# Kernel tuning notes

Measured on AMD Instinct MI355X. Metric: run time of the kernel, lower is better.

Reference implementation:

```python
import jax, jax.numpy as jnp
import numpy as np

B, L, D, H = 2, 2048, 512, 8
Dh = D // H


def setup_inputs() -> dict:
    key = jax.random.key(0)
    ks = jax.random.split(key, 12)
    def lin(i):
        W = jax.random.normal(ks[i], (D, D), dtype=jnp.float32) * (1.0 / np.sqrt(D))
        b = jax.random.normal(ks[i + 1], (D,), dtype=jnp.float32) * 0.02
        return W, b
    Wq, bq = lin(0)
    Wk, bk = lin(2)
    Wv, bv = lin(4)
    Wo, bo = lin(6)
    wave_real = jax.random.normal(ks[8], (B, L, D), dtype=jnp.float32)
    wave_imag = jax.random.normal(ks[9], (B, L, D), dtype=jnp.float32)
    return {"wave_real": wave_real, "wave_imag": wave_imag,
            "Wq": Wq, "bq": bq, "Wk": Wk, "bk": bk,
            "Wv": Wv, "bv": bv, "Wo": Wo, "bo": bo}


def _heads(x):
    # (B,L,D) -> (B,H,L,Dh)
    return x.reshape(B, L, H, Dh).transpose(0, 2, 1, 3)


def reference(wave_real, wave_imag, Wq, bq, Wk, bk, Wv, bv, Wo, bo):
    Qr = _heads(wave_real @ Wq.T + bq)
    Qi = _heads(wave_imag @ Wq.T + bq)
    Kr = _heads(wave_real @ Wk.T + bk)
    Ki = _heads(wave_imag @ Wk.T + bk)
    Vr = _heads(wave_real @ Wv.T + bv)
    Vi = _heads(wave_imag @ Wv.T + bv)

    inner_real = jnp.einsum('bhid,bhjd->bhij', Qr, Kr) + jnp.einsum('bhid,bhjd->bhij', Qi, Ki)
    inner_imag = jnp.einsum('bhid,bhjd->bhij', Qr, Ki) - jnp.einsum('bhid,bhjd->bhij', Qi, Kr)

    scores = (inner_real ** 2 + inner_imag ** 2) / np.sqrt(Dh).astype(np.float32)
    attention = jax.nn.softmax(scores, axis=-1)

    phase = jnp.arctan2(inner_imag, inner_real)
    ac = attention * jnp.cos(phase)  # (B,H,L,L)
    as_ = attention * jnp.sin(phase)

    # sum_j att_ij*(Vr_j*cos_ij - Vi_j*sin_ij) -- fused contraction, same math as
    # the original's materialized (B,H,L,L,Dh) rotate-then-sum.
    out_real = jnp.einsum('bhij,bhjd->bhid', ac, Vr) - jnp.einsum('bhij,bhjd->bhid', as_, Vi)
    out_imag = jnp.einsum('bhij,bhjd->bhid', as_, Vr) + jnp.einsum('bhij,bhjd->bhid', ac, Vi)

    out_real = out_real.transpose(0, 2, 1, 3).reshape(B, L, D)
    out_imag = out_imag.transpose(0, 2, 1, 3).reshape(B, L, D)
    return (out_real @ Wo.T + bo, out_imag @ Wo.T + bo, attention)
```

## Files before the change

kernel.cpp:

```cpp
#include <hip/hip_runtime.h>

typedef unsigned short u16;
typedef unsigned int   u32;
typedef __attribute__((ext_vector_type(4)))  u16   us4;
typedef __attribute__((ext_vector_type(8)))  u16   us8;
typedef __attribute__((ext_vector_type(8)))  short s8v;
typedef __attribute__((ext_vector_type(16))) float f32x16;

#define L_   2048
#define D_   512
#define H_   8
#define PE_  2097152ull

#define MATE    2097152ull
#define BHE     131072u
#define VT_OFF  33554432ull
#define ORH_OFF 41943040ull
#define ORL_OFF 46137344ull
#define OIH_OFF 50331648ull
#define OIL_OFF 54525952ull
#define LV_OFF  58720256ull

#define XRH_O 16777216ull
#define XRL_O 20971520ull
#define XIH_O 25165824ull
#define XIL_O 29360128ull

#define MFMA32(a,b,c) __builtin_amdgcn_mfma_f32_32x32x16_bf16(a,b,c,0,0,0)
#define ROWOF(r,hi) (((r)&3) + 8*((r)>>2) + 4*(hi))

__device__ __forceinline__ u16 f2bf(float x){
    u32 u = __float_as_uint(x);
    u += 0x7FFFu + ((u>>16)&1u);
    return (u16)(u>>16);
}
__device__ __forceinline__ float bf2f(u16 h){ return __uint_as_float(((u32)h)<<16); }

__global__ __launch_bounds__(256)
void split_prep_kernel(const float* __restrict__ wr, const float* __restrict__ wi,
                       unsigned char* __restrict__ outb)
{
    const int z = blockIdx.y;
    const float* src = z ? wi : wr;
    u16* hg = (u16*)(outb + (z ? XIH_O : XRH_O));
    u16* lg = (u16*)(outb + (z ? XIL_O : XRL_O));
    const size_t idx4 = ((size_t)blockIdx.x * 256 + threadIdx.x) * 4;
    float4 v = *(const float4*)&src[idx4];
    float vv[4] = { v.x, v.y, v.z, v.w };
    us4 h, l;
    #pragma unroll
    for (int c = 0; c < 4; ++c) {
        u16 hb = f2bf(vv[c]);
        h[c] = hb;
        l[c] = f2bf(vv[c] - bf2f(hb));
    }
    *(us4*)&hg[idx4] = h;
    *(us4*)&lg[idx4] = l;
}

__device__ __forceinline__ s8v ldfrag(const unsigned char* Lp, u32 matOff, u32 row, u32 colb)
{
    return *(const s8v*)(Lp + matOff + row*128u + (colb ^ ((row&7u)<<4)));
}
__device__ __forceinline__ void stage_qk(unsigned char* Lp, u32 matOff,
                                         const u16* __restrict__ g, int rowBase, int tid)
{
    const int ch = tid & 7;
    const int r0 = tid >> 3;
    #pragma unroll
    for (int rr = 0; rr < 2; ++rr) {
        u32 row = rr*32 + r0;
        us8 v = ((const us8*)(g + (size_t)(rowBase + row)*64))[ch];
        *(us8*)(Lp + matOff + row*128u + (((u32)ch<<4) ^ ((row&7u)<<4))) = v;
    }
}
__device__ __forceinline__ void stage_vt(unsigned char* Lp, u32 matOff,
                                         const u16* __restrict__ g, int j0, int tid, bool neg)
{
    const int ch = tid & 7;
    const int r0 = tid >> 3;
    #pragma unroll
    for (int rr = 0; rr < 2; ++rr) {
        u32 dh = rr*32 + r0;
        us8 v = ((const us8*)(g + (size_t)dh*2048 + j0))[ch];
        if (neg) v = v ^ (u16)0x8000u;
        *(us8*)(Lp + matOff + dh*128u + (((u32)ch<<4) ^ ((dh&7u)<<4))) = v;
    }
}

__global__ __launch_bounds__(256, 2)
void proj_mfma_kernel(const unsigned char* __restrict__ scr,
                      const float* __restrict__ Wq, const float* __restrict__ Wk,
                      const float* __restrict__ Wv,
                      const float* __restrict__ bq, const float* __restrict__ bk,
                      const float* __restrict__ bv,
                      u16* __restrict__ qk, u16* __restrict__ vt)
{
    const int z = blockIdx.z;
    const u16* Ah_g = (const u16*)(scr + ((z & 1) ? XIH_O : XRH_O));
    const u16* Al_g = (const u16*)(scr + ((z & 1) ? XIL_O : XRL_O));
    const int wsel = z >> 1;
    const float* Wf; const float* bias;
    if (wsel == 0)      { Wf = Wq; bias = bq; }
    else if (wsel == 1) { Wf = Wk; bias = bk; }
    else                { Wf = Wv; bias = bv; }
    const bool four = (wsel < 2);

    const int m0 = blockIdx.x * 128;
    const int n0 = blockIdx.y * 64;

    __shared__ __align__(16) unsigned char L[49152];
    enum : u32 { AH=0, AL=16384, BH=32768, BL=40960 };

    const int tid  = threadIdx.x;
    const int lane = tid & 63;
    const int wid  = tid >> 6;
    const int wr   = wid >> 1, wc = wid & 1;
    const int l31  = lane & 31;
    const int hi   = lane >> 5;
    const u32 rowA0 = (u32)(wr*64 + l31);
    const u32 rowB  = (u32)(wc*32 + l31);

    f32x16 c0, c1;
    #pragma unroll
    for (int r = 0; r < 16; ++r) { c0[r] = 0.f; c1[r] = 0.f; }

    const int ch = tid & 7, r0 = tid >> 3;

    for (int k0 = 0; k0 < 512; k0 += 64) {
        __syncthreads();
        #pragma unroll
        for (int rr = 0; rr < 4; ++rr) {
            u32 row = (u32)(rr*32 + r0);
            u32 dst = row*128u + (((u32)ch<<4) ^ ((row&7u)<<4));
            us8 vh = *(const us8*)(Ah_g + (size_t)(m0 + row)*512 + k0 + ch*8);
            *(us8*)(L + AH + dst) = vh;
            if (four) {
                us8 vl = *(const us8*)(Al_g + (size_t)(m0 + row)*512 + k0 + ch*8);
                *(us8*)(L + AL + dst) = vl;
            }
        }
        #pragma unroll
        for (int rr = 0; rr < 2; ++rr) {
            u32 row = (u32)(rr*32 + r0);
            const float* src = Wf + (size_t)(n0 + row)*512 + k0 + ch*8;
            float4 v0 = *(const float4*)src;
            float4 v1 = *(const float4*)(src + 4);
            float vv[8] = { v0.x,v0.y,v0.z,v0.w, v1.x,v1.y,v1.z,v1.w };
            us8 hv, lv;
            #pragma unroll
            for (int j = 0; j < 8; ++j) {
                u16 hb = f2bf(vv[j]);
                hv[j] = hb;
                lv[j] = f2bf(vv[j] - bf2f(hb));
            }
            u32 dst = row*128u + (((u32)ch<<4) ^ ((row&7u)<<4));
            *(us8*)(L + BH + dst) = hv;
            if (four) *(us8*)(L + BL + dst) = lv;
        }
        __syncthreads();

        #pragma unroll
        for (int ks = 0; ks < 4; ++ks) {
            u32 colb = (u32)(ks*32 + hi*16);
            s8v a0h = ldfrag(L, AH, rowA0,      colb);
            s8v a1h = ldfrag(L, AH, rowA0 + 32, colb);
            s8v bh_ = ldfrag(L, BH, rowB,       colb);
            c0 = MFMA32(a0h, bh_, c0);
            c1 = MFMA32(a1h, bh_, c1);
            if (four) {
                s8v a0l = ldfrag(L, AL, rowA0,      colb);
                s8v a1l = ldfrag(L, AL, rowA0 + 32, colb);
                s8v bl_ = ldfrag(L, BL, rowB,       colb);
                c0 = MFMA32(a0h, bl_, c0); c0 = MFMA32(a0l, bh_, c0); c0 = MFMA32(a0l, bl_, c0);
                c1 = MFMA32(a1h, bl_, c1); c1 = MFMA32(a1l, bh_, c1); c1 = MFMA32(a1l, bl_, c1);
            }
        }
    }

    const int n  = n0 + wc*32 + l31;
    const float bvv = bias[n];
    const int h  = n >> 6, dh = n & 63;

    if (z < 4) {
        u16* hg = qk + (size_t)(2*z)   * MATE;
        u16* lg = qk + (size_t)(2*z+1) * MATE;
        #pragma unroll
        for (int f = 0; f < 2; ++f) {
            const f32x16& c = f ? c1 : c0;
            #pragma unroll
            for (int r = 0; r < 16; ++r) {
                int m  = m0 + wr*64 + 32*f + ROWOF(r, hi);
                int b_ = m >> 11, i = m & 2047;
                size_t idx = (size_t)(b_*8 + h)*BHE + (size_t)i*64 + dh;
                float v = c[r] + bvv;
                u16 hb = f2bf(v);
                hg[idx] = hb;
                lg[idx] = f2bf(v - bf2f(hb));
            }
        }
    } else {
        u16* vg = vt + (size_t)(z & 1) * MATE;
        #pragma unroll
        for (int f = 0; f < 2; ++f) {
            const f32x16& c = f ? c1 : c0;
            #pragma unroll
            for (int g = 0; g < 4; ++g) {
                int mb = m0 + wr*64 + 32*f + 8*g + 4*hi;
                int b_ = mb >> 11, ib = mb & 2047;
                us4 pv;
                #pragma unroll
                for (int j = 0; j < 4; ++j) pv[j] = f2bf(c[4*g + j] + bvv);
                *(us4*)&vg[(size_t)(b_*8 + h)*BHE + (size_t)dh*2048 + ib] = pv;
            }
        }
    }
}

__global__ __launch_bounds__(256, 2)
void attn_mfma_kernel(const u16* __restrict__ qk,
                      const u16* __restrict__ vt,
                      float* __restrict__ attnbuf,
                      u16* __restrict__ orh, u16* __restrict__ orl,
                      u16* __restrict__ oih, u16* __restrict__ oil,
                      float* __restrict__ l_out)
{
    const int bh = blockIdx.x;
    const int i0 = blockIdx.y * 64;
    const int tid  = threadIdx.x;
    const int lane = tid & 63;
    const int wid  = tid >> 6;
    const int wr   = wid >> 1, wc = wid & 1;
    const int l31  = lane & 31;
    const int hi   = lane >> 5;
    const u32 rowA = wr*32 + l31;
    const u32 rowB = wc*32 + l31;

    __shared__ __align__(16) unsigned char L[81920];
    enum : u32 { QRH=0, QRL=8192, QIH=16384, QIL=24576,
                 KRH=32768, KRL=40960, KIH=49152, KIL=57344,
                 VRo=32768, VIo=40960, VNo=49152,
                 PAC=65536, PAS=73728 };

    const u16* qrh = qk + 0*MATE + (size_t)bh*BHE;
    const u16* qrl = qk + 1*MATE + (size_t)bh*BHE;
    const u16* qih = qk + 2*MATE + (size_t)bh*BHE;
    const u16* qil = qk + 3*MATE + (size_t)bh*BHE;
    const u16* krh = qk + 4*MATE + (size_t)bh*BHE;
    const u16* krl = qk + 5*MATE + (size_t)bh*BHE;
    const u16* kih = qk + 6*MATE + (size_t)bh*BHE;
    const u16* kil = qk + 7*MATE + (size_t)bh*BHE;
    const u16* vtr = vt + 0*MATE + (size_t)bh*BHE;
    const u16* vti = vt + 1*MATE + (size_t)bh*BHE;

    stage_qk(L, QRH, qrh, i0, tid);
    stage_qk(L, QRL, qrl, i0, tid);
    stage_qk(L, QIH, qih, i0, tid);
    stage_qk(L, QIL, qil, i0, tid);

    float mxv[16];
    #pragma unroll
    for (int r = 0; r < 16; ++r) mxv[r] = 0.f;

    for (int jp = 0; jp < 16; ++jp) {
        __syncthreads();
        stage_qk(L, KRH, krh, (2*jp)*64,     tid);
        stage_qk(L, KIH, kih, (2*jp)*64,     tid);
        stage_qk(L, KRL, krh, (2*jp+1)*64,   tid);
        stage_qk(L, KIL, kih, (2*jp+1)*64,   tid);
        __syncthreads();
        __builtin_amdgcn_s_setprio(1);
        #pragma unroll
        for (int half = 0; half < 2; ++half) {
            const u32 kR = half ? KRL : KRH;
            const u32 kI = half ? KIL : KIH;
            f32x16 ir, ip, in_;
            #pragma unroll
            for (int r = 0; r < 16; ++r) { ir[r]=0.f; ip[r]=0.f; in_[r]=0.f; }
            #pragma unroll
            for (int ks = 0; ks < 4; ++ks) {
                u32 colb = ks*32 + hi*16;
                s8v aR = ldfrag(L, QRH, rowA, colb);
                s8v aI = ldfrag(L, QIH, rowA, colb);
                s8v bR = ldfrag(L, kR,  rowB, colb);
                s8v bI = ldfrag(L, kI,  rowB, colb);
                ir  = MFMA32(aR, bR, ir);
                ir  = MFMA32(aI, bI, ir);
                ip  = MFMA32(aR, bI, ip);
                in_ = MFMA32(aI, bR, in_);
            }
            #pragma unroll
            for (int r = 0; r < 16; ++r) {
                float xr = ir[r], xi = ip[r] - in_[r];
                float q = xr*xr + xi*xi;
                mxv[r] = fmaxf(mxv[r], q * 0.125f);
            }
        }
        __builtin_amdgcn_s_setprio(0);
    }
    #pragma unroll
    for (int m = 1; m < 32; m <<= 1)
        #pragma unroll
        for (int r = 0; r < 16; ++r) mxv[r] = fmaxf(mxv[r], __shfl_xor(mxv[r], m));

    float* sc = (float*)(L + PAC);
    __syncthreads();
    #pragma unroll
    for (int r = 0; r < 16; ++r)
        if (l31 == r) sc[wc*64 + wr*32 + ROWOF(r,hi)] = mxv[r];
    __syncthreads();
    float mfin[16];
    #pragma unroll
    for (int r = 0; r < 16; ++r) {
        u32 row = wr*32 + ROWOF(r,hi);
        mfin[r] = fmaxf(sc[row], sc[64 + row]);
    }

    f32x16 ore, oim;
    float lp[16];
    #pragma unroll
    for (int r = 0; r < 16; ++r) { ore[r]=0.f; oim[r]=0.f; lp[r]=0.f; }

    for (int jt = 0; jt < 32; ++jt) {
        const int j0 = jt * 64;
        __syncthreads();
        stage_qk(L, KRH, krh, j0, tid);
        stage_qk(L, KRL, krl, j0, tid);
        stage_qk(L, KIH, kih, j0, tid);
        stage_qk(L, KIL, kil, j0, tid);
        __syncthreads();

        f32x16 ir, ip, in_;
        #pragma unroll
        for (int r = 0; r < 16; ++r) { ir[r]=0.f; ip[r]=0.f; in_[r]=0.f; }
        __builtin_amdgcn_s_setprio(1);
        #pragma unroll
        for (int ks = 0; ks < 4; ++ks) {
            u32 colb = ks*32 + hi*16;
            s8v aRH = ldfrag(L, QRH, rowA, colb);
            s8v aRL = ldfrag(L, QRL, rowA, colb);
            s8v aIH = ldfrag(L, QIH, rowA, colb);
            s8v aIL = ldfrag(L, QIL, rowA, colb);
            s8v bRH = ldfrag(L, KRH, rowB, colb);
            s8v bRL = ldfrag(L, KRL, rowB, colb);
            s8v bIH = ldfrag(L, KIH, rowB, colb);
            s8v bIL = ldfrag(L, KIL, rowB, colb);
            ir = MFMA32(aRH, bRH, ir); ir = MFMA32(aRH, bRL, ir); ir = MFMA32(aRL, bRH, ir);
            ir = MFMA32(aIH, bIH, ir); ir = MFMA32(aIH, bIL, ir); ir = MFMA32(aIL, bIH, ir);
            ip  = MFMA32(aRH, bIH, ip);  ip  = MFMA32(aRH, bIL, ip);  ip  = MFMA32(aRL, bIH, ip);
            in_ = MFMA32(aIH, bRH, in_); in_ = MFMA32(aIH, bRL, in_); in_ = MFMA32(aIL, bRH, in_);
        }
        __builtin_amdgcn_s_setprio(0);
        __syncthreads();
        stage_vt(L, VRo, vtr, j0, tid, false);
        stage_vt(L, VIo, vti, j0, tid, false);
        stage_vt(L, VNo, vti, j0, tid, true);

        float* arow = attnbuf + (size_t)bh*4194304ull + (size_t)i0*2048 + j0 + wc*32 + l31;
        #pragma unroll
        for (int r = 0; r < 16; ++r) {
            float xr = ir[r], xi = ip[r] - in_[r];
            float q  = fmaf(xr, xr, xi*xi);
            float e  = __expf(fmaf(q, 0.125f, -mfin[r]));
            lp[r] += e;
            float iv = rsqrtf(q);
            float t  = e * iv;
            float pc = (q > 0.f) ? xr*t : e;
            float ps = (q > 0.f) ? xi*t : 0.0f;
            u32 rowloc = wr*32 + ROWOF(r,hi);
            arow[(size_t)rowloc*2048] = e;
            u32 colb2 = (wc*32 + l31)*2;
            *(u16*)(L + PAC + rowloc*128u + (colb2 ^ ((rowloc&7u)<<4))) = f2bf(pc);
            *(u16*)(L + PAS + rowloc*128u + (colb2 ^ ((rowloc&7u)<<4))) = f2bf(ps);
        }
        __syncthreads();

        __builtin_amdgcn_s_setprio(1);
        #pragma unroll
        for (int ks = 0; ks < 4; ++ks) {
            u32 colb = ks*32 + hi*16;
            s8v aC = ldfrag(L, PAC, rowA, colb);
            s8v aS = ldfrag(L, PAS, rowA, colb);
            s8v vR = ldfrag(L, VRo, rowB, colb);
            s8v vI = ldfrag(L, VIo, rowB, colb);
            s8v vN = ldfrag(L, VNo, rowB, colb);
            ore = MFMA32(aC, vR, ore); ore = MFMA32(aS, vN, ore);
            oim = MFMA32(aS, vR, oim); oim = MFMA32(aC, vI, oim);
        }
        __builtin_amdgcn_s_setprio(0);
    }

    #pragma unroll
    for (int m = 1; m < 32; m <<= 1)
        #pragma unroll
        for (int r = 0; r < 16; ++r) lp[r] += __shfl_xor(lp[r], m);

    __syncthreads();
    #pragma unroll
    for (int r = 0; r < 16; ++r)
        if (l31 == r) sc[wc*64 + wr*32 + ROWOF(r,hi)] = lp[r];
    __syncthreads();

    const int b_ = bh >> 3, h = bh & 7;
    const size_t cb = (size_t)h*64 + wc*32 + l31;
    #pragma unroll
    for (int r = 0; r < 16; ++r) {
        u32 row = wr*32 + ROWOF(r,hi);
        float ls = sc[row] + sc[64 + row];
        if (wc == 0 && l31 == 0) l_out[(size_t)bh*2048 + i0 + row] = ls;
        float inv = 1.0f / ls;
        size_t idx = ((size_t)b_*2048 + i0 + row)*512 + cb;
        float vr = ore[r] * inv;
        float vi = oim[r] * inv;
        u16 hr = f2bf(vr); orh[idx] = hr; orl[idx] = f2bf(vr - bf2f(hr));
        u16 hw = f2bf(vi); oih[idx] = hw; oil[idx] = f2bf(vi - bf2f(hw));
    }
}

__global__ __launch_bounds__(256)
void scale_attn_kernel(float* __restrict__ attnbuf, const float* __restrict__ l)
{
    const size_t idx = (size_t)blockIdx.x * 256 + threadIdx.x;
    const size_t row = idx >> 9;
    const float inv = 1.f / l[row];
    float4* p = (float4*)attnbuf + idx;
    float4 v = *p;
    v.x *= inv; v.y *= inv; v.z *= inv; v.w *= inv;
    *p = v;
}

__global__ __launch_bounds__(256, 2)
void oproj_mfma_kernel(const unsigned char* __restrict__ wsb,
                       const float* __restrict__ Wo, const float* __restrict__ bo,
                       float* __restrict__ out)
{
    const int z = blockIdx.z;
    const u16* Ah_g = (const u16*)(wsb + (z ? OIH_OFF : ORH_OFF));
    const u16* Al_g = (const u16*)(wsb + (z ? OIL_OFF : ORL_OFF));
    float* outp = out + (size_t)z * PE_;

    const int m0 = blockIdx.x * 128;
    const int n0 = blockIdx.y * 64;

    __shared__ __align__(16) unsigned char L[49152];
    enum : u32 { AH=0, AL=16384, BH=32768, BL=40960 };

    const int tid  = threadIdx.x;
    const int lane = tid & 63;
    const int wid  = tid >> 6;
    const int wr   = wid >> 1, wc = wid & 1;
    const int l31  = lane & 31;
    const int hi   = lane >> 5;
    const u32 rowA0 = (u32)(wr*64 + l31);
    const u32 rowB  = (u32)(wc*32 + l31);

    f32x16 c0, c1;
    #pragma unroll
    for (int r = 0; r < 16; ++r) { c0[r] = 0.f; c1[r] = 0.f; }

    const int ch = tid & 7, r0 = tid >> 3;

    for (int k0 = 0; k0 < 512; k0 += 64) {
        __syncthreads();
        #pragma unroll
        for (int rr = 0; rr < 4; ++rr) {
            u32 row = (u32)(rr*32 + r0);
            u32 dst = row*128u + (((u32)ch<<4) ^ ((row&7u)<<4));
            us8 vh = *(const us8*)(Ah_g + (size_t)(m0 + row)*512 + k0 + ch*8);
            us8 vl = *(const us8*)(Al_g + (size_t)(m0 + row)*512 + k0 + ch*8);
            *(us8*)(L + AH + dst) = vh;
            *(us8*)(L + AL + dst) = vl;
        }
        #pragma unroll
        for (int rr = 0; rr < 2; ++rr) {
            u32 row = (u32)(rr*32 + r0);
            const float* src = Wo + (size_t)(n0 + row)*512 + k0 + ch*8;
            float4 v0 = *(const float4*)src;
            float4 v1 = *(const float4*)(src + 4);
            float vv[8] = { v0.x,v0.y,v0.z,v0.w, v1.x,v1.y,v1.z,v1.w };
            us8 hv, lv;
            #pragma unroll
            for (int j = 0; j < 8; ++j) {
                u16 hb = f2bf(vv[j]);
                hv[j] = hb;
                lv[j] = f2bf(vv[j] - bf2f(hb));
            }
            u32 dst = row*128u + (((u32)ch<<4) ^ ((row&7u)<<4));
            *(us8*)(L + BH + dst) = hv;
            *(us8*)(L + BL + dst) = lv;
        }
        __syncthreads();

        #pragma unroll
        for (int ks = 0; ks < 4; ++ks) {
            u32 colb = (u32)(ks*32 + hi*16);
            s8v a0h = ldfrag(L, AH, rowA0,      colb);
            s8v a1h = ldfrag(L, AH, rowA0 + 32, colb);
            s8v a0l = ldfrag(L, AL, rowA0,      colb);
            s8v a1l = ldfrag(L, AL, rowA0 + 32, colb);
            s8v bh_ = ldfrag(L, BH, rowB,       colb);
            s8v bl_ = ldfrag(L, BL, rowB,       colb);
            c0 = MFMA32(a0h, bh_, c0); c0 = MFMA32(a0h, bl_, c0); c0 = MFMA32(a0l, bh_, c0);
            c1 = MFMA32(a1h, bh_, c1); c1 = MFMA32(a1h, bl_, c1); c1 = MFMA32(a1l, bh_, c1);
        }
    }

    const int n = n0 + wc*32 + l31;
    const float bvv = bo[n];
    #pragma unroll
    for (int f = 0; f < 2; ++f) {
        const f32x16& c = f ? c1 : c0;
        #pragma unroll
        for (int r = 0; r < 16; ++r) {
            int m = m0 + wr*64 + 32*f + ROWOF(r, hi);
            outp[(size_t)m*512 + n] = c[r] + bvv;
        }
    }
}

extern "C" void kernel_launch(void* const* d_in, const int* in_sizes, int n_in,
                              void* d_out, int out_size, void* d_ws, size_t ws_size,
                              hipStream_t stream)
{
    const float* wave_real = (const float*)d_in[0];
    const float* wave_imag = (const float*)d_in[1];
    const float* Wq = (const float*)d_in[2]; const float* bq = (const float*)d_in[3];
    const float* Wk = (const float*)d_in[4]; const float* bk = (const float*)d_in[5];
    const float* Wv = (const float*)d_in[6]; const float* bv = (const float*)d_in[7];
    const float* Wo = (const float*)d_in[8]; const float* bo = (const float*)d_in[9];
    float* out = (float*)d_out;
    unsigned char* outb = (unsigned char*)d_out;
    unsigned char* wsb  = (unsigned char*)d_ws;

    float* attnbuf = out + 2*PE_;

    split_prep_kernel<<<dim3(2048, 2), dim3(256), 0, stream>>>(wave_real, wave_imag, outb);

    proj_mfma_kernel<<<dim3(32, 8, 6), dim3(256), 0, stream>>>(
        outb, Wq, Wk, Wv, bq, bk, bv,
        (u16*)wsb, (u16*)(wsb + VT_OFF));

    attn_mfma_kernel<<<dim3(16, 32), dim3(256), 0, stream>>>(
        (const u16*)wsb, (const u16*)(wsb + VT_OFF), attnbuf,
        (u16*)(wsb + ORH_OFF), (u16*)(wsb + ORL_OFF),
        (u16*)(wsb + OIH_OFF), (u16*)(wsb + OIL_OFF),
        (float*)(wsb + LV_OFF));

    scale_attn_kernel<<<dim3(65536), dim3(256), 0, stream>>>(
        attnbuf, (const float*)(wsb + LV_OFF));

    oproj_mfma_kernel<<<dim3(32, 8, 2), dim3(256), 0, stream>>>(
        wsb, Wo, bo, out);
}
```

Baseline: 370.1 us.

## Replace two-pass softmax max with online lazy-rescaled running max

After: 417.7 us. 1.13x slower.

```diff
diff --git a/kernel.cpp b/kernel.cpp
--- a/kernel.cpp
+++ b/kernel.cpp
@@ -19,15 +19,18 @@
 #define ORL_OFF 46137344ull
 #define OIH_OFF 50331648ull
 #define OIL_OFF 54525952ull
-#define LV_OFF  58720256ull
 
 #define XRH_O 16777216ull
 #define XRL_O 20971520ull
 #define XIH_O 25165824ull
 #define XIL_O 29360128ull
+#define MH_F  0ull
+#define LV_F  1048576ull
+#define MF_F  1081344ull
 
 #define MFMA32(a,b,c) __builtin_amdgcn_mfma_f32_32x32x16_bf16(a,b,c,0,0,0)
 #define ROWOF(r,hi) (((r)&3) + 8*((r)>>2) + 4*(hi))
+#define RTHR 20.0f
 
 __device__ __forceinline__ u16 f2bf(float x){
     u32 u = __float_as_uint(x);
@@ -223,7 +226,8 @@
                       float* __restrict__ attnbuf,
                       u16* __restrict__ orh, u16* __restrict__ orl,
                       u16* __restrict__ oih, u16* __restrict__ oil,
-                      float* __restrict__ l_out)
+                      float* __restrict__ mh, float* __restrict__ l_out,
+                      float* __restrict__ mf_out)
 {
     const int bh = blockIdx.x;
     const int i0 = blockIdx.y * 64;
@@ -241,6 +245,7 @@
                  KRH=32768, KRL=40960, KIH=49152, KIL=57344,
                  VRo=32768, VIo=40960, VNo=49152,
                  PAC=65536, PAS=73728 };
+    float* sc = (float*)(L + PAC);
 
     const u16* qrh = qk + 0*MATE + (size_t)bh*BHE;
     const u16* qrl = qk + 1*MATE + (size_t)bh*BHE;
@@ -258,68 +263,12 @@
     stage_qk(L, QIH, qih, i0, tid);
     stage_qk(L, QIL, qil, i0, tid);
 
-    float mxv[16];
-    #pragma unroll
-    for (int r = 0; r < 16; ++r) mxv[r] = 0.f;
-
-    for (int jp = 0; jp < 16; ++jp) {
-        __syncthreads();
-        stage_qk(L, KRH, krh, (2*jp)*64,     tid);
-        stage_qk(L, KIH, kih, (2*jp)*64,     tid);
-        stage_qk(L, KRL, krh, (2*jp+1)*64,   tid);
-        stage_qk(L, KIL, kih, (2*jp+1)*64,   tid);
-        __syncthreads();
-        __builtin_amdgcn_s_setprio(1);
-        #pragma unroll
-        for (int half = 0; half < 2; ++half) {
-            const u32 kR = half ? KRL : KRH;
-            const u32 kI = half ? KIL : KIH;
-            f32x16 ir, ip, in_;
-            #pragma unroll
-            for (int r = 0; r < 16; ++r) { ir[r]=0.f; ip[r]=0.f; in_[r]=0.f; }
-            #pragma unroll
-            for (int ks = 0; ks < 4; ++ks) {
-                u32 colb = ks*32 + hi*16;
-                s8v aR = ldfrag(L, QRH, rowA, colb);
-                s8v aI = ldfrag(L, QIH, rowA, colb);
-                s8v bR = ldfrag(L, kR,  rowB, colb);
-                s8v bI = ldfrag(L, kI,  rowB, colb);
-                ir  = MFMA32(aR, bR, ir);
-                ir  = MFMA32(aI, bI, ir);
-                ip  = MFMA32(aR, bI, ip);
-                in_ = MFMA32(aI, bR, in_);
-            }
-            #pragma unroll
-            for (int r = 0; r < 16; ++r) {
-                float xr = ir[r], xi = ip[r] - in_[r];
-                float q = xr*xr + xi*xi;
-                mxv[r] = fmaxf(mxv[r], q * 0.125f);
-            }
-        }
-        __builtin_amdgcn_s_setprio(0);
-    }
-    #pragma unroll
-    for (int m = 1; m < 32; m <<= 1)
-        #pragma unroll
-        for (int r = 0; r < 16; ++r) mxv[r] = fmaxf(mxv[r], __shfl_xor(mxv[r], m));
-
-    float* sc = (float*)(L + PAC);
-    __syncthreads();
-    #pragma unroll
-    for (int r = 0; r < 16; ++r)
-        if (l31 == r) sc[wc*64 + wr*32 + ROWOF(r,hi)] = mxv[r];
-    __syncthreads();
-    float mfin[16];
-    #pragma unroll
-    for (int r = 0; r < 16; ++r) {
-        u32 row = wr*32 + ROWOF(r,hi);
-        mfin[r] = fmaxf(sc[row], sc[64 + row]);
-    }
-
     f32x16 ore, oim;
-    float lp[16];
-    #pragma unroll
-    for (int r = 0; r < 16; ++r) { ore[r]=0.f; oim[r]=0.f; lp[r]=0.f; }
+    float lp[16], mreg[16];
+    #pragma unroll
+    for (int r = 0; r < 16; ++r) { ore[r]=0.f; oim[r]=0.f; lp[r]=0.f; mreg[r]=0.f; }
+
+    float* mhb = mh + (size_t)bh*65536;
 
     for (int jt = 0; jt < 32; ++jt) {
         const int j0 = jt * 64;
@@ -351,7 +300,42 @@
             in_ = MFMA32(aIH, bRH, in_); in_ = MFMA32(aIH, bRL, in_); in_ = MFMA32(aIL, bRH, in_);
         }
         __builtin_amdgcn_s_setprio(0);
-        __syncthreads();
+
+        f32x16 xi;
+        float tm[16];
+        #pragma unroll
+        for (int r = 0; r < 16; ++r) {
+            xi[r] = ip[r] - in_[r];
+            tm[r] = fmaf(ir[r], ir[r], xi[r]*xi[r]);
+        }
+        #pragma unroll
+        for (int m = 1; m < 32; m <<= 1)
+            #pragma unroll
+            for (int r = 0; r < 16; ++r) tm[r] = fmaxf(tm[r], __shfl_xor(tm[r], m));
+        if (l31 == 0) {
+            #pragma unroll
+            for (int r = 0; r < 16; ++r)
+                sc[(wr*32 + ROWOF(r,hi))*2 + wc] = tm[r];
+        }
+        __syncthreads();
+
+        #pragma unroll
+        for (int r = 0; r < 16; ++r) {
+            u32 row = wr*32 + ROWOF(r,hi);
+            float tmax = fmaxf(sc[row*2], sc[row*2 + 1]) * 0.125f;
+            if (tmax > mreg[r] + RTHR) {
+                float f = __expf(mreg[r] - tmax);
+                lp[r] *= f; ore[r] *= f; oim[r] *= f;
+                mreg[r] = tmax;
+            }
+        }
+        if (wc == 0 && l31 == 0) {
+            #pragma unroll
+            for (int r = 0; r < 16; ++r)
+                mhb[(size_t)jt*2048 + i0 + wr*32 + ROWOF(r,hi)] = mreg[r];
+        }
+        __syncthreads();
+
         stage_vt(L, VRo, vtr, j0, tid, false);
         stage_vt(L, VIo, vti, j0, tid, false);
         stage_vt(L, VNo, vti, j0, tid, true);
@@ -359,14 +343,14 @@
         float* arow = attnbuf + (size_t)bh*4194304ull + (size_t)i0*2048 + j0 + wc*32 + l31;
         #pragma unroll
         for (int r = 0; r < 16; ++r) {
-            float xr = ir[r], xi = ip[r] - in_[r];
-            float q  = fmaf(xr, xr, xi*xi);
-            float e  = __expf(fmaf(q, 0.125f, -mfin[r]));
+            float xr = ir[r], xv = xi[r];
+            float q  = fmaf(xr, xr, xv*xv);
+            float e  = __expf(fmaf(q, 0.125f, -mreg[r]));
             lp[r] += e;
             float iv = rsqrtf(q);
             float t  = e * iv;
             float pc = (q > 0.f) ? xr*t : e;
-            float ps = (q > 0.f) ? xi*t : 0.0f;
+            float ps = (q > 0.f) ? xv*t : 0.0f;
             u32 rowloc = wr*32 + ROWOF(r,hi);
             arow[(size_t)rowloc*2048] = e;
             u32 colb2 = (wc*32 + l31)*2;
@@ -396,9 +380,11 @@
         for (int r = 0; r < 16; ++r) lp[r] += __shfl_xor(lp[r], m);
 
     __syncthreads();
-    #pragma unroll
-    for (int r = 0; r < 16; ++r)
-        if (l31 == r) sc[wc*64 + wr*32 + ROWOF(r,hi)] = lp[r];
+    if (l31 == 0) {
+        #pragma unroll
+        for (int r = 0; r < 16; ++r)
+            sc[(wr*32 + ROWOF(r,hi))*2 + wc] = lp[r];
+    }
     __syncthreads();
 
     const int b_ = bh >> 3, h = bh & 7;
@@ -406,8 +392,11 @@
     #pragma unroll
     for (int r = 0; r < 16; ++r) {
         u32 row = wr*32 + ROWOF(r,hi);
-        float ls = sc[row] + sc[64 + row];
-        if (wc == 0 && l31 == 0) l_out[(size_t)bh*2048 + i0 + row] = ls;
+        float ls = sc[row*2] + sc[row*2 + 1];
+        if (wc == 0 && l31 == 0) {
+            l_out[(size_t)bh*2048 + i0 + row]  = ls;
+            mf_out[(size_t)bh*2048 + i0 + row] = mreg[r];
+        }
         float inv = 1.0f / ls;
         size_t idx = ((size_t)b_*2048 + i0 + row)*512 + cb;
         float vr = ore[r] * inv;
@@ -418,14 +407,21 @@
 }
 
 __global__ __launch_bounds__(256)
-void scale_attn_kernel(float* __restrict__ attnbuf, const float* __restrict__ l)
+void scale_attn_kernel(float* __restrict__ attnbuf, const float* __restrict__ l,
+                       const float* __restrict__ mf, const float* __restrict__ mh)
 {
     const size_t idx = (size_t)blockIdx.x * 256 + threadIdx.x;
-    const size_t row = idx >> 9;
-    const float inv = 1.f / l[row];
+    const size_t g   = idx * 4;
+    const size_t row = g >> 11;
+    const u32    col = (u32)(g & 2047);
+    const u32    jt  = col >> 6;
+    const size_t bh  = row >> 11;
+    const size_t i   = row & 2047;
+    const float  mhv = mh[(bh*32 + jt)*2048 + i];
+    const float  fac = __expf(mhv - mf[row]) * (1.0f / l[row]);
     float4* p = (float4*)attnbuf + idx;
     float4 v = *p;
-    v.x *= inv; v.y *= inv; v.z *= inv; v.w *= inv;
+    v.x *= fac; v.y *= fac; v.z *= fac; v.w *= fac;
     *p = v;
 }
 
@@ -533,6 +529,9 @@
     unsigned char* wsb  = (unsigned char*)d_ws;
 
     float* attnbuf = out + 2*PE_;
+    float* mh  = out + MH_F;
+    float* lv  = out + LV_F;
+    float* mfv = out + MF_F;
 
     split_prep_kernel<<<dim3(2048, 2), dim3(256), 0, stream>>>(wave_real, wave_imag, outb);
 
@@ -544,10 +543,9 @@
         (const u16*)wsb, (const u16*)(wsb + VT_OFF), attnbuf,
         (u16*)(wsb + ORH_OFF), (u16*)(wsb + ORL_OFF),
         (u16*)(wsb + OIH_OFF), (u16*)(wsb + OIL_OFF),
-        (float*)(wsb + LV_OFF));
-
-    scale_attn_kernel<<<dim3(65536), dim3(256), 0, stream>>>(
-        attnbuf, (const float*)(wsb + LV_OFF));
+        mh, lv, mfv);
+
+    scale_attn_kernel<<<dim3(65536), dim3(256), 0, stream>>>(attnbuf, lv, mfv, mh);
 
     oproj_mfma_kernel<<<dim3(32, 8, 2), dim3(256), 0, stream>>>(
         wsb, Wo, bo, out);
```

## Stage attention tiles via direct global-to-LDS loads with pre-swizzled global layout

Applied to the files above, without the earlier changes.

Result: no change. 364.6 us (-1.5%).

```diff
diff --git a/kernel.cpp b/kernel.cpp
--- a/kernel.cpp
+++ b/kernel.cpp
@@ -36,6 +36,33 @@
 }
 __device__ __forceinline__ float bf2f(u16 h){ return __uint_as_float(((u32)h)<<16); }
 
+__device__ __forceinline__ void glds16(const void* gsrc, void* ldst)
+{
+    __builtin_amdgcn_global_load_lds(
+        (const __attribute__((address_space(1))) u32*)(unsigned long long)gsrc,
+        (__attribute__((address_space(3))) u32*)(u32)(unsigned long long)ldst,
+        16, 0, 0);
+}
+__device__ __forceinline__ void glds_mat(unsigned char* Lp, u32 matOff,
+                                         const u16* g, int rowBase, int lane)
+{
+    const char* gb = (const char*)(g + (size_t)rowBase * 64);
+    #pragma unroll
+    for (int s = 0; s < 8; ++s)
+        glds16(gb + s*1024 + lane*16, Lp + matOff + s*1024);
+}
+__device__ __forceinline__ void glds_vt(unsigned char* Lp, u32 matOff,
+                                        const u16* g, int j0, int lane, int s0)
+{
+    #pragma unroll
+    for (int s = 0; s < 4; ++s) {
+        int seg = s0 + s;
+        int dh  = seg*8 + (lane >> 3);
+        const char* gp = (const char*)g + (size_t)dh*4096 + (size_t)j0*2 + (lane & 7)*16;
+        glds16(gp, Lp + matOff + seg*1024u);
+    }
+}
+
 __global__ __launch_bounds__(256)
 void split_prep_kernel(const float* __restrict__ wr, const float* __restrict__ wi,
                        unsigned char* __restrict__ outb)
@@ -61,31 +88,6 @@
 __device__ __forceinline__ s8v ldfrag(const unsigned char* Lp, u32 matOff, u32 row, u32 colb)
 {
     return *(const s8v*)(Lp + matOff + row*128u + (colb ^ ((row&7u)<<4)));
-}
-__device__ __forceinline__ void stage_qk(unsigned char* Lp, u32 matOff,
-                                         const u16* __restrict__ g, int rowBase, int tid)
-{
-    const int ch = tid & 7;
-    const int r0 = tid >> 3;
-    #pragma unroll
-    for (int rr = 0; rr < 2; ++rr) {
-        u32 row = rr*32 + r0;
-        us8 v = ((const us8*)(g + (size_t)(rowBase + row)*64))[ch];
-        *(us8*)(Lp + matOff + row*128u + (((u32)ch<<4) ^ ((row&7u)<<4))) = v;
-    }
-}
-__device__ __forceinline__ void stage_vt(unsigned char* Lp, u32 matOff,
-                                         const u16* __restrict__ g, int j0, int tid, bool neg)
-{
-    const int ch = tid & 7;
-    const int r0 = tid >> 3;
-    #pragma unroll
-    for (int rr = 0; rr < 2; ++rr) {
-        u32 dh = rr*32 + r0;
-        us8 v = ((const us8*)(g + (size_t)dh*2048 + j0))[ch];
-        if (neg) v = v ^ (u16)0x8000u;
-        *(us8*)(Lp + matOff + dh*128u + (((u32)ch<<4) ^ ((dh&7u)<<4))) = v;
-    }
 }
 
 __global__ __launch_bounds__(256, 2)
@@ -192,7 +194,7 @@
             for (int r = 0; r < 16; ++r) {
                 int m  = m0 + wr*64 + 32*f + ROWOF(r, hi);
                 int b_ = m >> 11, i = m & 2047;
-                size_t idx = (size_t)(b_*8 + h)*BHE + (size_t)i*64 + dh;
+                size_t idx = (size_t)(b_*8 + h)*BHE + (size_t)i*64 + (dh ^ ((i&7)<<3));
                 float v = c[r] + bvv;
                 u16 hb = f2bf(v);
                 hg[idx] = hb;
@@ -211,7 +213,8 @@
                 us4 pv;
                 #pragma unroll
                 for (int j = 0; j < 4; ++j) pv[j] = f2bf(c[4*g + j] + bvv);
-                *(us4*)&vg[(size_t)(b_*8 + h)*BHE + (size_t)dh*2048 + ib] = pv;
+                int ibs = ib ^ ((dh & 7) << 3);
+                *(us4*)&vg[(size_t)(b_*8 + h)*BHE + (size_t)dh*2048 + ibs] = pv;
             }
         }
     }
@@ -239,8 +242,9 @@
     __shared__ __align__(16) unsigned char L[81920];
     enum : u32 { QRH=0, QRL=8192, QIH=16384, QIL=24576,
                  KRH=32768, KRL=40960, KIH=49152, KIL=57344,
-                 VRo=32768, VIo=40960, VNo=49152,
+                 VRo=32768, VIo=40960,
                  PAC=65536, PAS=73728 };
+    float* sc = (float*)(L + PAC);
 
     const u16* qrh = qk + 0*MATE + (size_t)bh*BHE;
     const u16* qrl = qk + 1*MATE + (size_t)bh*BHE;
@@ -253,21 +257,21 @@
     const u16* vtr = vt + 0*MATE + (size_t)bh*BHE;
     const u16* vti = vt + 1*MATE + (size_t)bh*BHE;
 
-    stage_qk(L, QRH, qrh, i0, tid);
-    stage_qk(L, QRL, qrl, i0, tid);
-    stage_qk(L, QIH, qih, i0, tid);
-    stage_qk(L, QIL, qil, i0, tid);
+    {
+        const u16* qsrc = (wid == 0) ? qrh : (wid == 1) ? qrl : (wid == 2) ? qih : qil;
+        glds_mat(L, (u32)(wid * 8192), qsrc, i0, lane);
+    }
 
     float mxv[16];
     #pragma unroll
     for (int r = 0; r < 16; ++r) mxv[r] = 0.f;
 
+    const u16* s1src = (wid & 1) ? kih : krh;
+    const u32  s1off = 32768u + (u32)(wid & 1)*16384u + (u32)(wid >> 1)*8192u;
+
     for (int jp = 0; jp < 16; ++jp) {
         __syncthreads();
-        stage_qk(L, KRH, krh, (2*jp)*64,     tid);
-        stage_qk(L, KIH, kih, (2*jp)*64,     tid);
-        stage_qk(L, KRL, krh, (2*jp+1)*64,   tid);
-        stage_qk(L, KIL, kih, (2*jp+1)*64,   tid);
+        glds_mat(L, s1off, s1src, (2*jp + (wid >> 1))*64, lane);
         __syncthreads();
         __builtin_amdgcn_s_setprio(1);
         #pragma unroll
@@ -303,7 +307,6 @@
         #pragma unroll
         for (int r = 0; r < 16; ++r) mxv[r] = fmaxf(mxv[r], __shfl_xor(mxv[r], m));
 
-    float* sc = (float*)(L + PAC);
     __syncthreads();
     #pragma unroll
     for (int r = 0; r < 16; ++r)
@@ -321,13 +324,16 @@
     #pragma unroll
     for (int r = 0; r < 16; ++r) { ore[r]=0.f; oim[r]=0.f; lp[r]=0.f; }
 
+    const u16* s2src = (wid == 0) ? krh : (wid == 1) ? krl : (wid == 2) ? kih : kil;
+    const u32  s2off = 32768u + (u32)wid * 8192u;
+    const u16* vsrc  = (wid < 2) ? vtr : vti;
+    const u32  voff  = (wid < 2) ? VRo : VIo;
+    const int  vseg  = (wid & 1) * 4;
+
     for (int jt = 0; jt < 32; ++jt) {
         const int j0 = jt * 64;
         __syncthreads();
-        stage_qk(L, KRH, krh, j0, tid);
-        stage_qk(L, KRL, krl, j0, tid);
-        stage_qk(L, KIH, kih, j0, tid);
-        stage_qk(L, KIL, kil, j0, tid);
+        glds_mat(L, s2off, s2src, j0, lane);
         __syncthreads();
 
         f32x16 ir, ip, in_;
@@ -352,9 +358,8 @@
         }
         __builtin_amdgcn_s_setprio(0);
         __syncthreads();
-        stage_vt(L, VRo, vtr, j0, tid, false);
-        stage_vt(L, VIo, vti, j0, tid, false);
-        stage_vt(L, VNo, vti, j0, tid, true);
+
+        glds_vt(L, voff, vsrc, j0, lane, vseg);
 
         float* arow = attnbuf + (size_t)bh*4194304ull + (size_t)i0*2048 + j0 + wc*32 + l31;
         #pragma unroll
@@ -383,7 +388,7 @@
             s8v aS = ldfrag(L, PAS, rowA, colb);
             s8v vR = ldfrag(L, VRo, rowB, colb);
             s8v vI = ldfrag(L, VIo, rowB, colb);
-            s8v vN = ldfrag(L, VNo, rowB, colb);
+            s8v vN = vI ^ (short)0x8000;
             ore = MFMA32(aC, vR, ore); ore = MFMA32(aS, vN, ore);
             oim = MFMA32(aS, vR, oim); oim = MFMA32(aC, vI, oim);
         }
```
